# Kernel optimization log

Hardware: AMD Instinct MI355X
Metric: run time of the kernel (lower is better)

Reference implementation:

```python
import jax, jax.numpy as jnp
import numpy as np

D_IN, H, H1, H2 = 50, 64, 32, 1

def setup_inputs() -> dict:
    key = jax.random.key(0)
    ks = jax.random.split(key, 13)
    s = 1.0 / np.sqrt(H)
    u = lambda k, shp: jax.random.uniform(k, shp, jnp.float32, -s, s)
    x = jax.random.normal(ks[0], (512, 2048, D_IN), jnp.float32)
    return {
        "x": x,
        "W_ih0": u(ks[1], (H, D_IN)), "W_hh0": u(ks[2], (H, H)),
        "b_ih0": u(ks[3], (H,)),      "b_hh0": u(ks[4], (H,)),
        "W_ih1": u(ks[5], (H, H)),    "W_hh1": u(ks[6], (H, H)),
        "b_ih1": u(ks[7], (H,)),      "b_hh1": u(ks[8], (H,)),
        "W1": u(ks[9], (H1, H)),      "b1": u(ks[10], (H1,)),
        "W2": u(ks[11], (H2, H1)),    "b2": u(ks[12], (H2,)),
    }

def reference(x, W_ih0, W_hh0, b_ih0, b_hh0, W_ih1, W_hh1, b_ih1, b_hh1, W1, b1, W2, b2):
    B = x.shape[0]
    # Precompute input projections for layer 0 for all timesteps: [S, B, H]
    xt = jnp.swapaxes(x, 0, 1)  # [S, B, D_IN]
    x_proj0 = jnp.einsum('sbd,hd->sbh', xt, W_ih0) + b_ih0 + b_hh0

    h0 = jnp.zeros((B, H), x.dtype)

    def step(carry, xp):
        h1, h2 = carry
        h1 = jnp.tanh(xp + h1 @ W_hh0.T)
        h2 = jnp.tanh(h1 @ W_ih1.T + b_ih1 + h2 @ W_hh1.T + b_hh1)
        return (h1, h2), None

    (h1f, h2f), _ = jax.lax.scan(step, (h0, h0), x_proj0)
    hidden = jax.nn.relu(h2f @ W1.T + b1)
    return jax.nn.sigmoid(hidden @ W2.T + b2)
```

## Files before the change

kernel.cpp:

```cpp
#include <hip/hip_runtime.h>

#define S_LEN 2048
#define DIN   50
#define H     64

__device__ __forceinline__ float tanh_fast(float v) {
    float e = __expf(2.0f * v);
    return 1.0f - 2.0f * __builtin_amdgcn_rcpf(e + 1.0f);
}

__device__ __forceinline__ float sum4groups(float v) {
#if __has_builtin(__builtin_amdgcn_permlane16_swap) && __has_builtin(__builtin_amdgcn_permlane32_swap)
    typedef unsigned u2 __attribute__((ext_vector_type(2)));
    u2 r = __builtin_amdgcn_permlane16_swap(__float_as_uint(v), __float_as_uint(v), false, false);
    float s = __uint_as_float(r[0]) + __uint_as_float(r[1]);
    u2 t = __builtin_amdgcn_permlane32_swap(__float_as_uint(s), __float_as_uint(s), false, false);
    return __uint_as_float(t[0]) + __uint_as_float(t[1]);
#else
    v += __shfl_xor(v, 16, 64);
    v += __shfl_xor(v, 32, 64);
    return v;
#endif
}

__global__ __launch_bounds__(256, 2)
void rnn_fused(const float* __restrict__ x,
               const float* __restrict__ W_ih0, const float* __restrict__ W_hh0,
               const float* __restrict__ b_ih0, const float* __restrict__ b_hh0,
               const float* __restrict__ W_ih1, const float* __restrict__ W_hh1,
               const float* __restrict__ b_ih1, const float* __restrict__ b_hh1,
               const float* __restrict__ W1, const float* __restrict__ b1,
               const float* __restrict__ W2, const float* __restrict__ b2,
               float* __restrict__ out)
{
    const int b    = blockIdx.x;
    const int tid  = threadIdx.x;
    const int lane = tid & 63;
    const int w    = tid >> 6;
    const int j    = lane & 15;
    const int kg   = lane >> 4;
    const int outj = 16 * w + j;

    __shared__ __align__(16) float xs[2][4][16];
    __shared__ __align__(16) float h1s[H];
    __shared__ __align__(16) float h2s[H];

    float wx[13];
    #pragma unroll
    for (int i = 0; i < 13; ++i) {
        int c = 13 * kg + i;
        wx[i] = (c < DIN) ? W_ih0[outj * DIN + c] : 0.0f;
    }
    float whh0_l[16], wih1_l[16], whh1_l[16];
    #pragma unroll
    for (int i = 0; i < 16; ++i) {
        whh0_l[i] = W_hh0[outj * H + 16 * kg + i];
        wih1_l[i] = W_ih1[outj * H + 16 * kg + i];
        whh1_l[i] = W_hh1[outj * H + 16 * kg + i];
    }
    const float bias0 = b_ih0[outj] + b_hh0[outj];
    const float bias1 = b_ih1[outj] + b_hh1[outj];

    const float* __restrict__ xrow = x + (size_t)b * (size_t)(S_LEN * DIN);

    const int  sw   = tid >> 4, sj = tid & 15;
    const int  scol = 13 * sw + sj;
    const bool sval = (tid < 64) && (sj < 13) && (scol < DIN);

    if (tid < 64) xs[0][sw][sj] = sval ? xrow[scol] : 0.0f;
    float pfA = sval ? xrow[1 * DIN + scol] : 0.0f;
    float pfB = sval ? xrow[2 * DIN + scol] : 0.0f;

    float h1c[16], h2c[16];
    #pragma unroll
    for (int i = 0; i < 16; ++i) { h1c[i] = 0.0f; h2c[i] = 0.0f; }

    __syncthreads();

    float xacc;
    {
        float a0 = 0, a1 = 0, a2 = 0, a3 = 0;
        #pragma unroll
        for (int q = 0; q < 3; ++q) {
            float4 xv = *(const float4*)&xs[0][kg][4 * q];
            a0 = fmaf(xv.x, wx[4 * q + 0], a0);
            a1 = fmaf(xv.y, wx[4 * q + 1], a1);
            a2 = fmaf(xv.z, wx[4 * q + 2], a2);
            a3 = fmaf(xv.w, wx[4 * q + 3], a3);
        }
        a0 = fmaf(xs[0][kg][12], wx[12], a0);
        xacc = (a0 + a1) + (a2 + a3);
    }

    for (int s = 0; s < S_LEN; ++s) {
        const int nb = (s + 1) & 1;

        float a0 = xacc, a1 = 0, a2 = 0, a3 = 0;
        #pragma unroll
        for (int q = 0; q < 4; ++q) {
            a0 = fmaf(h1c[4 * q + 0], whh0_l[4 * q + 0], a0);
            a1 = fmaf(h1c[4 * q + 1], whh0_l[4 * q + 1], a1);
            a2 = fmaf(h1c[4 * q + 2], whh0_l[4 * q + 2], a2);
            a3 = fmaf(h1c[4 * q + 3], whh0_l[4 * q + 3], a3);
        }
        float h1n = tanh_fast(sum4groups((a0 + a1) + (a2 + a3)) + bias0);

        if (tid < 64) xs[nb][sw][sj] = pfA;
        pfA = pfB;
        pfB = (sval && (s + 3) < S_LEN) ? xrow[(size_t)(s + 3) * DIN + scol] : 0.0f;

        float c0 = 0, c1 = 0, c2 = 0, c3 = 0;
        #pragma unroll
        for (int q = 0; q < 4; ++q) {
            c0 = fmaf(h2c[4 * q + 0], whh1_l[4 * q + 0], c0);
            c1 = fmaf(h2c[4 * q + 1], whh1_l[4 * q + 1], c1);
            c2 = fmaf(h2c[4 * q + 2], whh1_l[4 * q + 2], c2);
            c3 = fmaf(h2c[4 * q + 3], whh1_l[4 * q + 3], c3);
        }

        if (kg == 0) h1s[16 * w + j] = h1n;
        __syncthreads();

        float h1nc[16];
        #pragma unroll
        for (int q = 0; q < 4; ++q)
            *(float4*)&h1nc[4 * q] = *(const float4*)&h1s[16 * kg + 4 * q];

        float xn0 = 0, xn1 = 0, xn2 = 0, xn3 = 0;
        #pragma unroll
        for (int q = 0; q < 3; ++q) {
            float4 xv = *(const float4*)&xs[nb][kg][4 * q];
            xn0 = fmaf(xv.x, wx[4 * q + 0], xn0);
            xn1 = fmaf(xv.y, wx[4 * q + 1], xn1);
            xn2 = fmaf(xv.z, wx[4 * q + 2], xn2);
            xn3 = fmaf(xv.w, wx[4 * q + 3], xn3);
        }
        xn0 = fmaf(xs[nb][kg][12], wx[12], xn0);

        #pragma unroll
        for (int q = 0; q < 4; ++q) {
            c0 = fmaf(h1nc[4 * q + 0], wih1_l[4 * q + 0], c0);
            c1 = fmaf(h1nc[4 * q + 1], wih1_l[4 * q + 1], c1);
            c2 = fmaf(h1nc[4 * q + 2], wih1_l[4 * q + 2], c2);
            c3 = fmaf(h1nc[4 * q + 3], wih1_l[4 * q + 3], c3);
        }
        float h2n = tanh_fast(sum4groups((c0 + c1) + (c2 + c3)) + bias1);

        if (kg == 0) h2s[16 * w + j] = h2n;
        __syncthreads();

        #pragma unroll
        for (int q = 0; q < 4; ++q)
            *(float4*)&h2c[4 * q] = *(const float4*)&h2s[16 * kg + 4 * q];

        #pragma unroll
        for (int i = 0; i < 16; ++i) h1c[i] = h1nc[i];
        xacc = (xn0 + xn1) + (xn2 + xn3);
    }

    if (tid < 64) {
        float hv = 0.0f;
        if (lane < 32) {
            float acc = b1[lane];
            #pragma unroll
            for (int k = 0; k < H; ++k)
                acc = fmaf(h2s[k], W1[lane * H + k], acc);
            hv = fmaxf(acc, 0.0f) * W2[lane];
        }
        #pragma unroll
        for (int off = 32; off; off >>= 1)
            hv += __shfl_xor(hv, off, 64);
        if (lane == 0)
            out[b] = 1.0f / (1.0f + __expf(-(hv + b2[0])));
    }
}

extern "C" void kernel_launch(void* const* d_in, const int* in_sizes, int n_in,
                              void* d_out, int out_size, void* d_ws, size_t ws_size,
                              hipStream_t stream) {
    const float* x     = (const float*)d_in[0];
    const float* W_ih0 = (const float*)d_in[1];
    const float* W_hh0 = (const float*)d_in[2];
    const float* b_ih0 = (const float*)d_in[3];
    const float* b_hh0 = (const float*)d_in[4];
    const float* W_ih1 = (const float*)d_in[5];
    const float* W_hh1 = (const float*)d_in[6];
    const float* b_ih1 = (const float*)d_in[7];
    const float* b_hh1 = (const float*)d_in[8];
    const float* W1    = (const float*)d_in[9];
    const float* b1    = (const float*)d_in[10];
    const float* W2    = (const float*)d_in[11];
    const float* b2    = (const float*)d_in[12];
    float* out = (float*)d_out;

    rnn_fused<<<dim3(512), dim3(256), 0, stream>>>(
        x, W_ih0, W_hh0, b_ih0, b_hh0,
        W_ih1, W_hh1, b_ih1, b_hh1,
        W1, b1, W2, b2, out);
}
```

Baseline: 1.107 ms.

## Pipeline RNN layers across wave groups with one barrier per timestep

The block grows to 512 threads. Four waves compute layer 0 at step t while four other waves compute layer 1 at step t-1, using double-buffered shared hidden states, so each timestep needs one barrier instead of two. This wavefront pipelining shortens the serial critical path per step and halves the register weight load per thread. tanh also switches to a raw exp2 builtin. The cost is twice the threads per block and a fixed occupancy setting of 4 waves per EU, which may limit how many blocks can be resident at once.

```diff
diff --git a/kernel.cpp b/kernel.cpp
--- a/kernel.cpp
+++ b/kernel.cpp
@@ -5,17 +5,17 @@
 #define H     64
 
 __device__ __forceinline__ float tanh_fast(float v) {
-    float e = __expf(2.0f * v);
+    float e = __builtin_amdgcn_exp2f(v * 2.885390082f);
     return 1.0f - 2.0f * __builtin_amdgcn_rcpf(e + 1.0f);
 }
 
-__device__ __forceinline__ float sum4groups(float v) {
+__device__ __forceinline__ float red4(float v) {
 #if __has_builtin(__builtin_amdgcn_permlane16_swap) && __has_builtin(__builtin_amdgcn_permlane32_swap)
     typedef unsigned u2 __attribute__((ext_vector_type(2)));
     u2 r = __builtin_amdgcn_permlane16_swap(__float_as_uint(v), __float_as_uint(v), false, false);
     float s = __uint_as_float(r[0]) + __uint_as_float(r[1]);
-    u2 t = __builtin_amdgcn_permlane32_swap(__float_as_uint(s), __float_as_uint(s), false, false);
-    return __uint_as_float(t[0]) + __uint_as_float(t[1]);
+    u2 q = __builtin_amdgcn_permlane32_swap(__float_as_uint(s), __float_as_uint(s), false, false);
+    return __uint_as_float(q[0]) + __uint_as_float(q[1]);
 #else
     v += __shfl_xor(v, 16, 64);
     v += __shfl_xor(v, 32, 64);
@@ -23,7 +23,8 @@
 #endif
 }
 
-__global__ __launch_bounds__(256, 2)
+__global__ __launch_bounds__(512)
+__attribute__((amdgpu_waves_per_eu(4, 4)))
 void rnn_fused(const float* __restrict__ x,
                const float* __restrict__ W_ih0, const float* __restrict__ W_hh0,
                const float* __restrict__ b_ih0, const float* __restrict__ b_hh0,
@@ -36,127 +37,118 @@
     const int b    = blockIdx.x;
     const int tid  = threadIdx.x;
     const int lane = tid & 63;
-    const int w    = tid >> 6;
+    const int w    = __builtin_amdgcn_readfirstlane(tid >> 6);
+    const bool isA = (w < 4);
+    const int wr   = isA ? w : w - 4;
     const int j    = lane & 15;
     const int kg   = lane >> 4;
-    const int outj = 16 * w + j;
+    const int outj = 16 * wr + j;
 
     __shared__ __align__(16) float xs[2][4][16];
-    __shared__ __align__(16) float h1s[H];
-    __shared__ __align__(16) float h2s[H];
+    __shared__ __align__(16) float h1s[2][H];
+    __shared__ __align__(16) float h2s[2][H];
 
-    float wx[13];
-    #pragma unroll
-    for (int i = 0; i < 13; ++i) {
-        int c = 13 * kg + i;
-        wx[i] = (c < DIN) ? W_ih0[outj * DIN + c] : 0.0f;
+    float arrP[16], arrQ[16];
+    if (isA) {
+        #pragma unroll
+        for (int i = 0; i < 16; ++i) {
+            int c = 13 * kg + i;
+            arrP[i] = (i < 13 && c < DIN) ? W_ih0[outj * DIN + c] : 0.0f;
+            arrQ[i] = W_hh0[outj * H + 16 * kg + i];
+        }
+    } else {
+        #pragma unroll
+        for (int i = 0; i < 16; ++i) {
+            arrP[i] = W_ih1[outj * H + 16 * kg + i];
+            arrQ[i] = W_hh1[outj * H + 16 * kg + i];
+        }
     }
-    float whh0_l[16], wih1_l[16], whh1_l[16];
-    #pragma unroll
-    for (int i = 0; i < 16; ++i) {
-        whh0_l[i] = W_hh0[outj * H + 16 * kg + i];
-        wih1_l[i] = W_ih1[outj * H + 16 * kg + i];
-        whh1_l[i] = W_hh1[outj * H + 16 * kg + i];
-    }
-    const float bias0 = b_ih0[outj] + b_hh0[outj];
-    const float bias1 = b_ih1[outj] + b_hh1[outj];
+    const float bias = isA ? (b_ih0[outj] + b_hh0[outj])
+                           : (b_ih1[outj] + b_hh1[outj]);
 
     const float* __restrict__ xrow = x + (size_t)b * (size_t)(S_LEN * DIN);
 
-    const int  sw   = tid >> 4, sj = tid & 15;
-    const int  scol = 13 * sw + sj;
-    const bool sval = (tid < 64) && (sj < 13) && (scol < DIN);
+    const int  scol = 13 * kg + j;
+    const bool sval = (tid < 64) && (j < 13) && (scol < DIN);
 
-    if (tid < 64) xs[0][sw][sj] = sval ? xrow[scol] : 0.0f;
-    float pfA = sval ? xrow[1 * DIN + scol] : 0.0f;
+    if (tid < 64) xs[0][kg][j] = sval ? xrow[scol] : 0.0f;
+    float pfA = sval ? xrow[DIN + scol] : 0.0f;
     float pfB = sval ? xrow[2 * DIN + scol] : 0.0f;
+    const float* xpf = xrow + 3 * DIN + scol;
 
-    float h1c[16], h2c[16];
-    #pragma unroll
-    for (int i = 0; i < 16; ++i) { h1c[i] = 0.0f; h2c[i] = 0.0f; }
-
+    if (tid < 64) { h1s[1][lane] = 0.0f; h2s[1][lane] = 0.0f; }
     __syncthreads();
 
-    float xacc;
-    {
-        float a0 = 0, a1 = 0, a2 = 0, a3 = 0;
-        #pragma unroll
-        for (int q = 0; q < 3; ++q) {
-            float4 xv = *(const float4*)&xs[0][kg][4 * q];
-            a0 = fmaf(xv.x, wx[4 * q + 0], a0);
-            a1 = fmaf(xv.y, wx[4 * q + 1], a1);
-            a2 = fmaf(xv.z, wx[4 * q + 2], a2);
-            a3 = fmaf(xv.w, wx[4 * q + 3], a3);
+    auto iter = [&](int t, int cur, int prv) {
+        if (isA) {
+            if (t < S_LEN) {
+                float s1[16], s2[16];
+                #pragma unroll
+                for (int q = 0; q < 4; ++q)
+                    *(float4*)&s1[4 * q] = *(const float4*)&xs[cur][kg][4 * q];
+                #pragma unroll
+                for (int q = 0; q < 4; ++q)
+                    *(float4*)&s2[4 * q] = *(const float4*)&h1s[prv][16 * kg + 4 * q];
+                float a0 = 0, a1 = 0, a2 = 0, a3 = 0;
+                #pragma unroll
+                for (int q = 0; q < 4; ++q) {
+                    a0 = fmaf(s1[4 * q + 0], arrP[4 * q + 0], a0);
+                    a1 = fmaf(s1[4 * q + 1], arrP[4 * q + 1], a1);
+                    a2 = fmaf(s1[4 * q + 2], arrP[4 * q + 2], a2);
+                    a3 = fmaf(s1[4 * q + 3], arrP[4 * q + 3], a3);
+                }
+                #pragma unroll
+                for (int q = 0; q < 4; ++q) {
+                    a0 = fmaf(s2[4 * q + 0], arrQ[4 * q + 0], a0);
+                    a1 = fmaf(s2[4 * q + 1], arrQ[4 * q + 1], a1);
+                    a2 = fmaf(s2[4 * q + 2], arrQ[4 * q + 2], a2);
+                    a3 = fmaf(s2[4 * q + 3], arrQ[4 * q + 3], a3);
+                }
+                float h1n = tanh_fast(red4((a0 + a1) + (a2 + a3)) + bias);
+                if (kg == 0) h1s[cur][outj] = h1n;
+                if (tid < 64) xs[prv][kg][j] = pfA;
+                pfA = pfB;
+                pfB = (sval && (t + 3) < S_LEN) ? *xpf : 0.0f;
+                xpf += DIN;
+            }
+        } else {
+            if (t >= 1) {
+                float s1[16], s2[16];
+                #pragma unroll
+                for (int q = 0; q < 4; ++q)
+                    *(float4*)&s1[4 * q] = *(const float4*)&h1s[prv][16 * kg + 4 * q];
+                #pragma unroll
+                for (int q = 0; q < 4; ++q)
+                    *(float4*)&s2[4 * q] = *(const float4*)&h2s[cur][16 * kg + 4 * q];
+                float c0 = 0, c1 = 0, c2 = 0, c3 = 0;
+                #pragma unroll
+                for (int q = 0; q < 4; ++q) {
+                    c0 = fmaf(s1[4 * q + 0], arrP[4 * q + 0], c0);
+                    c1 = fmaf(s1[4 * q + 1], arrP[4 * q + 1], c1);
+                    c2 = fmaf(s1[4 * q + 2], arrP[4 * q + 2], c2);
+                    c3 = fmaf(s1[4 * q + 3], arrP[4 * q + 3], c3);
+                }
+                #pragma unroll
+                for (int q = 0; q < 4; ++q) {
+                    c0 = fmaf(s2[4 * q + 0], arrQ[4 * q + 0], c0);
+                    c1 = fmaf(s2[4 * q + 1], arrQ[4 * q + 1], c1);
+                    c2 = fmaf(s2[4 * q + 2], arrQ[4 * q + 2], c2);
+                    c3 = fmaf(s2[4 * q + 3], arrQ[4 * q + 3], c3);
+                }
+                float h2n = tanh_fast(red4((c0 + c1) + (c2 + c3)) + bias);
+                if (kg == 0) h2s[prv][outj] = h2n;
+            }
         }
-        a0 = fmaf(xs[0][kg][12], wx[12], a0);
-        xacc = (a0 + a1) + (a2 + a3);
+    };
+
+    for (int t = 0; t < S_LEN; t += 2) {
+        iter(t, 0, 1);
+        __syncthreads();
+        iter(t + 1, 1, 0);
+        __syncthreads();
     }
-
-    for (int s = 0; s < S_LEN; ++s) {
-        const int nb = (s + 1) & 1;
-
-        float a0 = xacc, a1 = 0, a2 = 0, a3 = 0;
-        #pragma unroll
-        for (int q = 0; q < 4; ++q) {
-            a0 = fmaf(h1c[4 * q + 0], whh0_l[4 * q + 0], a0);
-            a1 = fmaf(h1c[4 * q + 1], whh0_l[4 * q + 1], a1);
-            a2 = fmaf(h1c[4 * q + 2], whh0_l[4 * q + 2], a2);
-            a3 = fmaf(h1c[4 * q + 3], whh0_l[4 * q + 3], a3);
-        }
-        float h1n = tanh_fast(sum4groups((a0 + a1) + (a2 + a3)) + bias0);
-
-        if (tid < 64) xs[nb][sw][sj] = pfA;
-        pfA = pfB;
-        pfB = (sval && (s + 3) < S_LEN) ? xrow[(size_t)(s + 3) * DIN + scol] : 0.0f;
-
-        float c0 = 0, c1 = 0, c2 = 0, c3 = 0;
-        #pragma unroll
-        for (int q = 0; q < 4; ++q) {
-            c0 = fmaf(h2c[4 * q + 0], whh1_l[4 * q + 0], c0);
-            c1 = fmaf(h2c[4 * q + 1], whh1_l[4 * q + 1], c1);
-            c2 = fmaf(h2c[4 * q + 2], whh1_l[4 * q + 2], c2);
-            c3 = fmaf(h2c[4 * q + 3], whh1_l[4 * q + 3], c3);
-        }
-
-        if (kg == 0) h1s[16 * w + j] = h1n;
-        __syncthreads();
-
-        float h1nc[16];
-        #pragma unroll
-        for (int q = 0; q < 4; ++q)
-            *(float4*)&h1nc[4 * q] = *(const float4*)&h1s[16 * kg + 4 * q];
-
-        float xn0 = 0, xn1 = 0, xn2 = 0, xn3 = 0;
-        #pragma unroll
-        for (int q = 0; q < 3; ++q) {
-            float4 xv = *(const float4*)&xs[nb][kg][4 * q];
-            xn0 = fmaf(xv.x, wx[4 * q + 0], xn0);
-            xn1 = fmaf(xv.y, wx[4 * q + 1], xn1);
-            xn2 = fmaf(xv.z, wx[4 * q + 2], xn2);
-            xn3 = fmaf(xv.w, wx[4 * q + 3], xn3);
-        }
-        xn0 = fmaf(xs[nb][kg][12], wx[12], xn0);
-
-        #pragma unroll
-        for (int q = 0; q < 4; ++q) {
-            c0 = fmaf(h1nc[4 * q + 0], wih1_l[4 * q + 0], c0);
-            c1 = fmaf(h1nc[4 * q + 1], wih1_l[4 * q + 1], c1);
-            c2 = fmaf(h1nc[4 * q + 2], wih1_l[4 * q + 2], c2);
-            c3 = fmaf(h1nc[4 * q + 3], wih1_l[4 * q + 3], c3);
-        }
-        float h2n = tanh_fast(sum4groups((c0 + c1) + (c2 + c3)) + bias1);
-
-        if (kg == 0) h2s[16 * w + j] = h2n;
-        __syncthreads();
-
-        #pragma unroll
-        for (int q = 0; q < 4; ++q)
-            *(float4*)&h2c[4 * q] = *(const float4*)&h2s[16 * kg + 4 * q];
-
-        #pragma unroll
-        for (int i = 0; i < 16; ++i) h1c[i] = h1nc[i];
-        xacc = (xn0 + xn1) + (xn2 + xn3);
-    }
+    iter(S_LEN, 0, 1);
+    __syncthreads();
 
     if (tid < 64) {
         float hv = 0.0f;
@@ -164,7 +156,7 @@
             float acc = b1[lane];
             #pragma unroll
             for (int k = 0; k < H; ++k)
-                acc = fmaf(h2s[k], W1[lane * H + k], acc);
+                acc = fmaf(h2s[1][k], W1[lane * H + k], acc);
             hv = fmaxf(acc, 0.0f) * W2[lane];
         }
         #pragma unroll
@@ -193,7 +185,7 @@
     const float* b2    = (const float*)d_in[12];
     float* out = (float*)d_out;
 
-    rnn_fused<<<dim3(512), dim3(256), 0, stream>>>(
+    rnn_fused<<<dim3(512), dim3(512), 0, stream>>>(
         x, W_ih0, W_hh0, b_ih0, b_hh0,
         W_ih1, W_hh1, b_ih1, b_hh1,
         W1, b1, W2, b2, out);
```

Result: no change. 1.087 ms (-1.8%).

## Stage x in 32-timestep LDS chunks instead of per-step register prefetch

Applied to the files above, without the earlier changes.

Replaces the per-step global prefetch pipeline (two register-held lookahead rows plus a double-buffered LDS slot) with bulk loading of 32 timesteps of x into shared memory. The serial recurrence loop then reads the input projection only from LDS, removing a global load and predicated store from each step. It also switches tanh to a direct exp2 builtin and pins waves-per-EU to 2. The trade-off is an unhidden global-load stall plus a barrier at the start of every 32-step chunk.

```diff
diff --git a/kernel.cpp b/kernel.cpp
--- a/kernel.cpp
+++ b/kernel.cpp
@@ -3,19 +3,21 @@
 #define S_LEN 2048
 #define DIN   50
 #define H     64
+#define XB    32
+#define XEL   (XB * 52)
 
 __device__ __forceinline__ float tanh_fast(float v) {
-    float e = __expf(2.0f * v);
+    float e = __builtin_amdgcn_exp2f(v * 2.885390082f);
     return 1.0f - 2.0f * __builtin_amdgcn_rcpf(e + 1.0f);
 }
 
-__device__ __forceinline__ float sum4groups(float v) {
+__device__ __forceinline__ float red4(float v) {
 #if __has_builtin(__builtin_amdgcn_permlane16_swap) && __has_builtin(__builtin_amdgcn_permlane32_swap)
     typedef unsigned u2 __attribute__((ext_vector_type(2)));
     u2 r = __builtin_amdgcn_permlane16_swap(__float_as_uint(v), __float_as_uint(v), false, false);
     float s = __uint_as_float(r[0]) + __uint_as_float(r[1]);
-    u2 t = __builtin_amdgcn_permlane32_swap(__float_as_uint(s), __float_as_uint(s), false, false);
-    return __uint_as_float(t[0]) + __uint_as_float(t[1]);
+    u2 q = __builtin_amdgcn_permlane32_swap(__float_as_uint(s), __float_as_uint(s), false, false);
+    return __uint_as_float(q[0]) + __uint_as_float(q[1]);
 #else
     v += __shfl_xor(v, 16, 64);
     v += __shfl_xor(v, 32, 64);
@@ -23,7 +25,8 @@
 #endif
 }
 
-__global__ __launch_bounds__(256, 2)
+__global__ __launch_bounds__(256)
+__attribute__((amdgpu_waves_per_eu(2, 2)))
 void rnn_fused(const float* __restrict__ x,
                const float* __restrict__ W_ih0, const float* __restrict__ W_hh0,
                const float* __restrict__ b_ih0, const float* __restrict__ b_hh0,
@@ -41,7 +44,7 @@
     const int kg   = lane >> 4;
     const int outj = 16 * w + j;
 
-    __shared__ __align__(16) float xs[2][4][16];
+    __shared__ __align__(16) float xb[XB][4][16];
     __shared__ __align__(16) float h1s[H];
     __shared__ __align__(16) float h2s[H];
 
@@ -63,99 +66,97 @@
 
     const float* __restrict__ xrow = x + (size_t)b * (size_t)(S_LEN * DIN);
 
-    const int  sw   = tid >> 4, sj = tid & 15;
-    const int  scol = 13 * sw + sj;
-    const bool sval = (tid < 64) && (sj < 13) && (scol < DIN);
-
-    if (tid < 64) xs[0][sw][sj] = sval ? xrow[scol] : 0.0f;
-    float pfA = sval ? xrow[1 * DIN + scol] : 0.0f;
-    float pfB = sval ? xrow[2 * DIN + scol] : 0.0f;
-
     float h1c[16], h2c[16];
     #pragma unroll
     for (int i = 0; i < 16; ++i) { h1c[i] = 0.0f; h2c[i] = 0.0f; }
 
-    __syncthreads();
-
-    float xacc;
-    {
-        float a0 = 0, a1 = 0, a2 = 0, a3 = 0;
+    float xacc = 0.0f;
+
+    for (int T = 0; T < S_LEN; T += XB) {
         #pragma unroll
-        for (int q = 0; q < 3; ++q) {
-            float4 xv = *(const float4*)&xs[0][kg][4 * q];
-            a0 = fmaf(xv.x, wx[4 * q + 0], a0);
-            a1 = fmaf(xv.y, wx[4 * q + 1], a1);
-            a2 = fmaf(xv.z, wx[4 * q + 2], a2);
-            a3 = fmaf(xv.w, wx[4 * q + 3], a3);
-        }
-        a0 = fmaf(xs[0][kg][12], wx[12], a0);
-        xacc = (a0 + a1) + (a2 + a3);
-    }
-
-    for (int s = 0; s < S_LEN; ++s) {
-        const int nb = (s + 1) & 1;
-
-        float a0 = xacc, a1 = 0, a2 = 0, a3 = 0;
-        #pragma unroll
-        for (int q = 0; q < 4; ++q) {
-            a0 = fmaf(h1c[4 * q + 0], whh0_l[4 * q + 0], a0);
-            a1 = fmaf(h1c[4 * q + 1], whh0_l[4 * q + 1], a1);
-            a2 = fmaf(h1c[4 * q + 2], whh0_l[4 * q + 2], a2);
-            a3 = fmaf(h1c[4 * q + 3], whh0_l[4 * q + 3], a3);
-        }
-        float h1n = tanh_fast(sum4groups((a0 + a1) + (a2 + a3)) + bias0);
-
-        if (tid < 64) xs[nb][sw][sj] = pfA;
-        pfA = pfB;
-        pfB = (sval && (s + 3) < S_LEN) ? xrow[(size_t)(s + 3) * DIN + scol] : 0.0f;
-
-        float c0 = 0, c1 = 0, c2 = 0, c3 = 0;
-        #pragma unroll
-        for (int q = 0; q < 4; ++q) {
-            c0 = fmaf(h2c[4 * q + 0], whh1_l[4 * q + 0], c0);
-            c1 = fmaf(h2c[4 * q + 1], whh1_l[4 * q + 1], c1);
-            c2 = fmaf(h2c[4 * q + 2], whh1_l[4 * q + 2], c2);
-            c3 = fmaf(h2c[4 * q + 3], whh1_l[4 * q + 3], c3);
-        }
-
-        if (kg == 0) h1s[16 * w + j] = h1n;
+        for (int r = 0; r < 7; ++r) {
+            int f = tid + 256 * r;
+            if (f < XEL) {
+                int t   = f / 52;
+                int rem = f - 52 * t;
+                int c   = rem / 13;
+                int jj  = rem - 13 * c;
+                int col = 13 * c + jj;
+                xb[t][c][jj] = (col < DIN) ? xrow[(size_t)(T + t) * DIN + col] : 0.0f;
+            }
+        }
         __syncthreads();
 
-        float h1nc[16];
-        #pragma unroll
-        for (int q = 0; q < 4; ++q)
-            *(float4*)&h1nc[4 * q] = *(const float4*)&h1s[16 * kg + 4 * q];
-
-        float xn0 = 0, xn1 = 0, xn2 = 0, xn3 = 0;
-        #pragma unroll
-        for (int q = 0; q < 3; ++q) {
-            float4 xv = *(const float4*)&xs[nb][kg][4 * q];
-            xn0 = fmaf(xv.x, wx[4 * q + 0], xn0);
-            xn1 = fmaf(xv.y, wx[4 * q + 1], xn1);
-            xn2 = fmaf(xv.z, wx[4 * q + 2], xn2);
-            xn3 = fmaf(xv.w, wx[4 * q + 3], xn3);
-        }
-        xn0 = fmaf(xs[nb][kg][12], wx[12], xn0);
-
-        #pragma unroll
-        for (int q = 0; q < 4; ++q) {
-            c0 = fmaf(h1nc[4 * q + 0], wih1_l[4 * q + 0], c0);
-            c1 = fmaf(h1nc[4 * q + 1], wih1_l[4 * q + 1], c1);
-            c2 = fmaf(h1nc[4 * q + 2], wih1_l[4 * q + 2], c2);
-            c3 = fmaf(h1nc[4 * q + 3], wih1_l[4 * q + 3], c3);
-        }
-        float h2n = tanh_fast(sum4groups((c0 + c1) + (c2 + c3)) + bias1);
-
-        if (kg == 0) h2s[16 * w + j] = h2n;
-        __syncthreads();
-
-        #pragma unroll
-        for (int q = 0; q < 4; ++q)
-            *(float4*)&h2c[4 * q] = *(const float4*)&h2s[16 * kg + 4 * q];
-
-        #pragma unroll
-        for (int i = 0; i < 16; ++i) h1c[i] = h1nc[i];
-        xacc = (xn0 + xn1) + (xn2 + xn3);
+        {
+            const float4* xq = (const float4*)&xb[0][kg][0];
+            float4 x0 = xq[0], x1 = xq[1], x2 = xq[2];
+            float a0 = x0.x * wx[0], a1 = x0.y * wx[1], a2 = x0.z * wx[2], a3 = x0.w * wx[3];
+            a0 = fmaf(x1.x, wx[4], a0);  a1 = fmaf(x1.y, wx[5], a1);
+            a2 = fmaf(x1.z, wx[6], a2);  a3 = fmaf(x1.w, wx[7], a3);
+            a0 = fmaf(x2.x, wx[8], a0);  a1 = fmaf(x2.y, wx[9], a1);
+            a2 = fmaf(x2.z, wx[10], a2); a3 = fmaf(x2.w, wx[11], a3);
+            a0 = fmaf(xb[0][kg][12], wx[12], a0);
+            xacc = (a0 + a1) + (a2 + a3);
+        }
+
+        #pragma unroll 2
+        for (int u = 0; u < XB; ++u) {
+            float a0 = xacc, a1 = 0.0f, a2 = 0.0f, a3 = 0.0f;
+            #pragma unroll
+            for (int q = 0; q < 4; ++q) {
+                a0 = fmaf(h1c[4 * q + 0], whh0_l[4 * q + 0], a0);
+                a1 = fmaf(h1c[4 * q + 1], whh0_l[4 * q + 1], a1);
+                a2 = fmaf(h1c[4 * q + 2], whh0_l[4 * q + 2], a2);
+                a3 = fmaf(h1c[4 * q + 3], whh0_l[4 * q + 3], a3);
+            }
+            float h1n = tanh_fast(red4((a0 + a1) + (a2 + a3)) + bias0);
+
+            float c0 = 0.0f, c1 = 0.0f, c2 = 0.0f, c3 = 0.0f;
+            #pragma unroll
+            for (int q = 0; q < 4; ++q) {
+                c0 = fmaf(h2c[4 * q + 0], whh1_l[4 * q + 0], c0);
+                c1 = fmaf(h2c[4 * q + 1], whh1_l[4 * q + 1], c1);
+                c2 = fmaf(h2c[4 * q + 2], whh1_l[4 * q + 2], c2);
+                c3 = fmaf(h2c[4 * q + 3], whh1_l[4 * q + 3], c3);
+            }
+
+            if (kg == 0) h1s[outj] = h1n;
+            __syncthreads();
+
+            *(float4*)&h1c[0]  = *(const float4*)&h1s[16 * kg + 0];
+            *(float4*)&h1c[4]  = *(const float4*)&h1s[16 * kg + 4];
+            *(float4*)&h1c[8]  = *(const float4*)&h1s[16 * kg + 8];
+            *(float4*)&h1c[12] = *(const float4*)&h1s[16 * kg + 12];
+
+            {
+                const float4* xq = (const float4*)&xb[(u + 1) & (XB - 1)][kg][0];
+                float4 x0 = xq[0], x1 = xq[1], x2 = xq[2];
+                float xn0 = x0.x * wx[0], xn1 = x0.y * wx[1], xn2 = x0.z * wx[2], xn3 = x0.w * wx[3];
+                xn0 = fmaf(x1.x, wx[4], xn0);  xn1 = fmaf(x1.y, wx[5], xn1);
+                xn2 = fmaf(x1.z, wx[6], xn2);  xn3 = fmaf(x1.w, wx[7], xn3);
+                xn0 = fmaf(x2.x, wx[8], xn0);  xn1 = fmaf(x2.y, wx[9], xn1);
+                xn2 = fmaf(x2.z, wx[10], xn2); xn3 = fmaf(x2.w, wx[11], xn3);
+                xn0 = fmaf(xb[(u + 1) & (XB - 1)][kg][12], wx[12], xn0);
+                xacc = (xn0 + xn1) + (xn2 + xn3);
+            }
+
+            #pragma unroll
+            for (int q = 0; q < 4; ++q) {
+                c0 = fmaf(h1c[4 * q + 0], wih1_l[4 * q + 0], c0);
+                c1 = fmaf(h1c[4 * q + 1], wih1_l[4 * q + 1], c1);
+                c2 = fmaf(h1c[4 * q + 2], wih1_l[4 * q + 2], c2);
+                c3 = fmaf(h1c[4 * q + 3], wih1_l[4 * q + 3], c3);
+            }
+            float h2n = tanh_fast(red4((c0 + c1) + (c2 + c3)) + bias1);
+
+            if (kg == 0) h2s[outj] = h2n;
+            __syncthreads();
+
+            *(float4*)&h2c[0]  = *(const float4*)&h2s[16 * kg + 0];
+            *(float4*)&h2c[4]  = *(const float4*)&h2s[16 * kg + 4];
+            *(float4*)&h2c[8]  = *(const float4*)&h2s[16 * kg + 8];
+            *(float4*)&h2c[12] = *(const float4*)&h2s[16 * kg + 12];
+        }
     }
 
     if (tid < 64) {
```

Result: faster. 1.045 ms (-5.5%).
